# Kernel optimization log

Hardware: AMD Instinct MI355X
Metric: run time of the kernel (lower is better)

## Reference

```python
import jax, jax.numpy as jnp
import numpy as np

N_NODES = 50000
N_EDGES = 800000
N_GRAPHS = 128
IN_CH = 31
HID = 64
EPS = 1e-5


def _glorot(key, shape, scale=0.05):
    return jax.random.normal(key, shape, dtype=jnp.float32) * scale


def setup_inputs() -> dict:
    key = jax.random.key(0)
    ks = jax.random.split(key, 16)
    x = jax.random.normal(ks[0], (N_NODES, IN_CH), dtype=jnp.float32)
    edge_index = jax.random.randint(ks[1], (2, N_EDGES), 0, N_NODES, dtype=jnp.int32)
    batch = jnp.sort(jax.random.randint(ks[2], (N_NODES,), 0, N_GRAPHS, dtype=jnp.int32))
    params = {
        "t": jnp.ones((1,), dtype=jnp.float32),  # shared learnable softmax temperature
        "W1r": _glorot(ks[3], (HID, IN_CH)), "b1": jnp.zeros((HID,), jnp.float32), "W1s": _glorot(ks[4], (HID, IN_CH)),
        "W2r": _glorot(ks[5], (HID, HID)),  "b2": jnp.zeros((HID,), jnp.float32), "W2s": _glorot(ks[6], (HID, HID)),
        "W3r": _glorot(ks[7], (HID, HID)),  "b3": jnp.zeros((HID,), jnp.float32), "W3s": _glorot(ks[8], (HID, HID)),
        "Wl1": _glorot(ks[9], (2 * HID, 3 * HID)), "bl1": jnp.zeros((2 * HID,), jnp.float32),
        "Wl2": _glorot(ks[10], (HID // 2, 2 * HID)), "bl2": jnp.zeros((HID // 2,), jnp.float32),
    }
    return {"x": x, "edge_index": edge_index, "batch": batch, **params}


def _softmax_aggr(m, dst, t, n):
    # segment-softmax over incoming edges, per channel: alpha = softmax(t*m | dst)
    logits = m * t  # [E, C]
    mx = jax.ops.segment_max(logits, dst, num_segments=n)  # [N, C]
    e = jnp.exp(logits - mx[dst])
    denom = jax.ops.segment_sum(e, dst, num_segments=n)
    alpha = e / denom[dst]
    return jax.ops.segment_sum(m * alpha, dst, num_segments=n)  # [N, C]


def _graph_conv(x, src, dst, t, Wr, br, Ws):
    # PyG GraphConv: out = lin_rel(aggr_j x_j) + lin_root(x); lin_root has no bias
    m = x[src]  # gather [E, C]
    aggr = _softmax_aggr(m, dst, t, x.shape[0])
    return aggr @ Wr.T + br + x @ Ws.T


def _instance_norm(x):
    # torch InstanceNorm1d on [N, C] input -> normalize each row over feature dim
    mu = jnp.mean(x, axis=1, keepdims=True)
    var = jnp.mean((x - mu) ** 2, axis=1, keepdims=True)
    return (x - mu) / jnp.sqrt(var + EPS)


def reference(x, edge_index, batch, t, W1r, b1, W1s, W2r, b2, W2s, W3r, b3, W3s, Wl1, bl1, Wl2, bl2):
    src, dst = edge_index[0], edge_index[1]
    x1 = jax.nn.relu(_instance_norm(_graph_conv(x, src, dst, t, W1r, b1, W1s)))
    x2 = jax.nn.relu(_instance_norm(_graph_conv(x1, src, dst, t, W2r, b2, W2s)))
    x3 = jax.nn.relu(_instance_norm(_graph_conv(x2, src, dst, t, W3r, b3, W3s)))
    h1 = jax.ops.segment_max(x1, batch, num_segments=N_GRAPHS)
    h2 = jax.ops.segment_max(x2, batch, num_segments=N_GRAPHS)
    h3 = jax.ops.segment_max(x3, batch, num_segments=N_GRAPHS)
    h = jnp.concatenate([h1, h2, h3], axis=1)  # [G, 3*HID]
    z = jax.nn.relu(h @ Wl1.T + bl1)  # dropout is identity in eval mode
    z = z @ Wl2.T + bl2
    norm = jnp.maximum(jnp.linalg.norm(z, axis=1, keepdims=True), 1e-12)
    return z / norm
```

## Files before the change

### kernel.cpp

```cpp
#include <hip/hip_runtime.h>
#include <hip/hip_fp16.h>

#define N_NODES 50000
#define N_EDGES 800000
#define N_GRAPHS 128
#define IN_CH 31
#define HID 64

typedef __attribute__((ext_vector_type(8))) short short8;
typedef __attribute__((ext_vector_type(8))) unsigned short ushort8;
typedef __attribute__((ext_vector_type(4))) float floatx4;

__device__ inline unsigned f2bf(float f) {
    union { float f; unsigned u; } v; v.f = f;
    unsigned r = v.u + 0x7fff + ((v.u >> 16) & 1);
    return r >> 16;
}
__device__ inline void pack4(short* p, float4 v) {
    unsigned lo = f2bf(v.x) | (f2bf(v.y) << 16);
    unsigned hi = f2bf(v.z) | (f2bf(v.w) << 16);
    *(uint2*)p = make_uint2(lo, hi);
}
__device__ inline unsigned packEP(float E, float P) {
    __half2 h = __floats2half2_rn(E, P);
    return *(unsigned*)&h;
}
__device__ inline float2 unpackEP(unsigned u) {
    __half2 h = *(__half2*)&u;
    return __half22float2(h);
}

__global__ void prep_kernel(const float* __restrict__ x, const float* __restrict__ tptr,
                            unsigned short* __restrict__ xbf, unsigned* __restrict__ EP0,
                            int nN) {
    int i = blockIdx.x * 256 + threadIdx.x;
    if (i >= nN * 32) return;
    int node = i >> 5, c = i & 31;
    if (c < IN_CH) {
        float xv = x[node * IN_CH + c];
        xbf[node * IN_CH + c] = (unsigned short)f2bf(xv);
        float tval = tptr[0];
        float E = __expf(tval * xv);
        EP0[i] = packEP(E, xv * E);
    } else {
        EP0[i] = 0;
    }
}


#define BKT_SHIFT 7
#define BKT_MAX 512
#define CHUNK 8192
#define CAP 2560

__global__ void bucket_scatter_kernel(const int* __restrict__ src,
                                      const int* __restrict__ dst,
                                      int* __restrict__ bucket_cnt,
                                      unsigned* __restrict__ ebuf, int e, int nb) {
    __shared__ int bins[BKT_MAX];
    __shared__ int base[BKT_MAX];
    __shared__ int lcur[BKT_MAX];
    int tid = threadIdx.x;
    int i0 = blockIdx.x * CHUNK;
    int i1 = i0 + CHUNK; if (i1 > e) i1 = e;
    for (int k = tid; k < nb; k += 256) { bins[k] = 0; lcur[k] = 0; }
    __syncthreads();
    for (int j = i0 + tid; j < i1; j += 256)
        atomicAdd(&bins[dst[j] >> BKT_SHIFT], 1);
    __syncthreads();
    for (int k = tid; k < nb; k += 256)
        if (bins[k]) base[k] = atomicAdd(&bucket_cnt[k], bins[k]);
    __syncthreads();
    for (int j = i0 + tid; j < i1; j += 256) {
        int ss = src[j], dd = dst[j];
        int b = dd >> BKT_SHIFT;
        int p = atomicAdd(&lcur[b], 1);
        ebuf[(size_t)b * CAP + base[b] + p] = (unsigned)ss | ((unsigned)(dd & 127) << 16);
    }
}

__global__ void bucket_csr_kernel(const unsigned* __restrict__ ebuf,
                                  const int* __restrict__ bucket_cnt,
                                  int* __restrict__ row_ptr, int* __restrict__ deg,
                                  int* __restrict__ csr_src, int nN) {
    __shared__ int nh[128];
    __shared__ int s[128];
    __shared__ int ncur[128];
    int tid = threadIdx.x;
    int b = blockIdx.x;
    int cnt = bucket_cnt[b];
    size_t boff = (size_t)b * CAP;
    int node0 = b << BKT_SHIFT;
    if (tid < 128) nh[tid] = 0;
    __syncthreads();
    for (int j = tid; j < cnt; j += 256)
        atomicAdd(&nh[ebuf[boff + j] >> 16], 1);
    __syncthreads();
    int v = (tid < 128) ? nh[tid] : 0;
    if (tid < 128) s[tid] = v;
    __syncthreads();
    for (int off = 1; off < 128; off <<= 1) {
        int u = (tid < 128 && tid >= off) ? s[tid - off] : 0;
        __syncthreads();
        if (tid < 128) s[tid] += u;
        __syncthreads();
    }
    if (tid < 128 && node0 + tid < nN) {
        int excl = (int)boff + s[tid] - v;
        row_ptr[node0 + tid] = excl;
        deg[node0 + tid] = v;
        ncur[tid] = excl;
    }
    __syncthreads();
    for (int j = tid; j < cnt; j += 256) {
        unsigned ed = ebuf[boff + j];
        int pos = atomicAdd(&ncur[ed >> 16], 1);
        csr_src[pos] = (int)(ed & 0xFFFF);
    }
}


template <int C_IN>
__global__ void __launch_bounds__(256, 8) aggr_kernel(
        const unsigned* __restrict__ EP, const unsigned short* __restrict__ xin,
        const int* __restrict__ row_ptr, const int* __restrict__ deg,
        const int* __restrict__ csr_src,
        unsigned short* __restrict__ aRowsB, int n) {
    int w = threadIdx.x >> 6, l = threadIdx.x & 63;
    int d = blockIdx.x * 4 + w;
    if (d >= n) return;
    int beg = __builtin_amdgcn_readfirstlane(row_ptr[d]);
    int dg  = __builtin_amdgcn_readfirstlane(deg[d]);
    int end = beg + dg;
    int half = l >> 5;

    if constexpr (C_IN == 64) {
        int co = l & 31;
        float2 num2 = {0.f, 0.f}, den2 = {0.f, 0.f};
        int base = beg;
        for (; base + 64 <= end; base += 64) {
            int sidx = csr_src[base + l];
            #pragma unroll
            for (int j = 0; j < 64; j += 16) {
                uint2 v[8];
                #pragma unroll
                for (int p = 0; p < 8; ++p) {
                    int sa = __builtin_amdgcn_readlane(sidx, j + 2 * p);
                    int sb = __builtin_amdgcn_readlane(sidx, j + 2 * p + 1);
                    int s  = half ? sb : sa;
                    v[p] = *(const uint2*)&EP[(size_t)s * 64 + 2 * co];
                }
                #pragma unroll
                for (int p = 0; p < 8; ++p) {
                    float2 e0 = unpackEP(v[p].x);
                    float2 e1 = unpackEP(v[p].y);
                    den2.x += e0.x; num2.x += e0.y;
                    den2.y += e1.x; num2.y += e1.y;
                }
            }
        }
        int rem = end - base;
        if (rem > 0) {
            int sidx = csr_src[base + ((l < rem) ? l : 0)];
            for (int j = 0; j < rem; j += 16) {
                uint2 v[8];
                #pragma unroll
                for (int p = 0; p < 8; ++p) {
                    int ja = j + 2 * p;     if (ja >= rem) ja = rem - 1;
                    int jb = j + 2 * p + 1; if (jb >= rem) jb = rem - 1;
                    int sa = __builtin_amdgcn_readlane(sidx, ja);
                    int sb = __builtin_amdgcn_readlane(sidx, jb);
                    int s  = half ? sb : sa;
                    v[p] = *(const uint2*)&EP[(size_t)s * 64 + 2 * co];
                }
                #pragma unroll
                for (int p = 0; p < 8; ++p) {
                    float m = (j + 2 * p + half < rem) ? 1.f : 0.f;
                    float2 e0 = unpackEP(v[p].x);
                    float2 e1 = unpackEP(v[p].y);
                    den2.x = fmaf(e0.x, m, den2.x); num2.x = fmaf(e0.y, m, num2.x);
                    den2.y = fmaf(e1.x, m, den2.y); num2.y = fmaf(e1.y, m, num2.y);
                }
            }
        }
        num2.x += __shfl_xor(num2.x, 32);
        num2.y += __shfl_xor(num2.y, 32);
        den2.x += __shfl_xor(den2.x, 32);
        den2.y += __shfl_xor(den2.y, 32);
        float nx = __shfl(num2.x, l >> 1);
        float ny = __shfl(num2.y, l >> 1);
        float dx = __shfl(den2.x, l >> 1);
        float dy = __shfl(den2.y, l >> 1);
        float num = (l & 1) ? ny : nx;
        float den = (l & 1) ? dy : dx;
        float aggr = (dg > 0 && den > 0.f) ? num / den : 0.f;
        aRowsB[(size_t)d * 64 + l] = (unsigned short)f2bf(aggr);
    } else {
        int ch = l & 31;
        int chc = (ch < C_IN) ? ch : (C_IN - 1);
        float num = 0.f, den = 0.f;
        int base = beg;
        for (; base + 64 <= end; base += 64) {
            int sidx = csr_src[base + l];
            #pragma unroll
            for (int j = 0; j < 64; j += 16) {
                unsigned v[8];
                #pragma unroll
                for (int p = 0; p < 8; ++p) {
                    int sa = __builtin_amdgcn_readlane(sidx, j + 2 * p);
                    int sb = __builtin_amdgcn_readlane(sidx, j + 2 * p + 1);
                    int s  = half ? sb : sa;
                    v[p] = EP[(size_t)s * 32 + chc];
                }
                #pragma unroll
                for (int p = 0; p < 8; ++p) {
                    float2 e = unpackEP(v[p]);
                    den += e.x;
                    num += e.y;
                }
            }
        }
        int rem = end - base;
        if (rem > 0) {
            int sidx = csr_src[base + ((l < rem) ? l : 0)];
            for (int j = 0; j < rem; j += 16) {
                unsigned v[8];
                #pragma unroll
                for (int p = 0; p < 8; ++p) {
                    int ja = j + 2 * p;     if (ja >= rem) ja = rem - 1;
                    int jb = j + 2 * p + 1; if (jb >= rem) jb = rem - 1;
                    int sa = __builtin_amdgcn_readlane(sidx, ja);
                    int sb = __builtin_amdgcn_readlane(sidx, jb);
                    int s  = half ? sb : sa;
                    v[p] = EP[(size_t)s * 32 + chc];
                }
                #pragma unroll
                for (int p = 0; p < 8; ++p) {
                    float m = (j + 2 * p + half < rem) ? 1.f : 0.f;
                    float2 e = unpackEP(v[p]);
                    den = fmaf(e.x, m, den);
                    num = fmaf(e.y, m, num);
                }
            }
        }
        num += __shfl_xor(num, 32);
        den += __shfl_xor(den, 32);
        float aggr = (dg > 0 && den > 0.f) ? num / den : 0.f;
        unsigned short outv;
        if (l < C_IN)               outv = (unsigned short)f2bf(aggr);
        else if (l < 2 * C_IN)      outv = xin[(size_t)d * C_IN + (l - C_IN)];
        else                        outv = 0;
        aRowsB[(size_t)d * 64 + l] = outv;
    }
}


template <int C_IN, bool WEP>
__global__ void __launch_bounds__(256, 4) transform_kernel(
        const unsigned short* __restrict__ aRowsB, const unsigned short* __restrict__ yprev,
        const int* __restrict__ batch,
        const float* __restrict__ Wr, const float* __restrict__ br,
        const float* __restrict__ Ws, const float* __restrict__ tptr,
        unsigned short* __restrict__ yout, unsigned* __restrict__ EPout,
        float* __restrict__ hmax, int n) {
    constexpr int K_TOT = (C_IN == 64) ? 128 : 64;
    constexpr int KP    = K_TOT + 8;
    constexpr int KS    = K_TOT / 32;
    constexpr int ABSH  = 2 * 64 * KP;
    constexpr int CSH   = 64 * 68 * 2;
    constexpr int SMSH  = (ABSH > CSH) ? ABSH : CSH;

    __shared__ short smem[SMSH];
    short* sA = smem;
    short* sB = smem + 64 * KP;
    float* sC = (float*)smem;

    int tid = threadIdx.x;
    int nb = blockIdx.x * 64;

    if constexpr (C_IN == 64) {
        for (int idx = tid; idx < 64 * 16; idx += 256) {
            int row = idx >> 4, c8 = idx & 15;
            int node = nb + row; if (node >= n) node = n - 1;
            ushort8 v = (c8 < 8) ? ((const ushort8*)(aRowsB + (size_t)node * 64))[c8]
                                 : ((const ushort8*)(yprev + (size_t)node * 64))[c8 - 8];
            *(ushort8*)&sA[row * KP + c8 * 8] = v;
        }
        for (int idx = tid; idx < 64 * 32; idx += 256) {
            int nr = idx >> 5, c4 = idx & 31;
            float4 v = (c4 < 16) ? ((const float4*)(Wr + nr * 64))[c4]
                                 : ((const float4*)(Ws + nr * 64))[c4 - 16];
            pack4(&sB[nr * KP + c4 * 4], v);
        }
    } else {
        for (int idx = tid; idx < 64 * 8; idx += 256) {
            int row = idx >> 3, c8 = idx & 7;
            int node = nb + row; if (node >= n) node = n - 1;
            ushort8 v = ((const ushort8*)(aRowsB + (size_t)node * 64))[c8];
            *(ushort8*)&sA[row * KP + c8 * 8] = v;
        }
        for (int idx = tid; idx < 64 * 64; idx += 256) {
            int nr = idx >> 6, k = idx & 63;
            float v = (k < C_IN) ? Wr[nr * C_IN + k]
                    : (k < 2 * C_IN) ? Ws[nr * C_IN + (k - C_IN)] : 0.f;
            sB[nr * KP + k] = (short)f2bf(v);
        }
    }
    __syncthreads();

    int w = tid >> 6, l = tid & 63;
    int m = l & 15;
    int q = l >> 4;
    floatx4 acc[4] = {{0.f,0.f,0.f,0.f},{0.f,0.f,0.f,0.f},
                      {0.f,0.f,0.f,0.f},{0.f,0.f,0.f,0.f}};
    const short* aBase = &sA[(w * 16 + m) * KP + q * 8];
    #pragma unroll 2
    for (int s = 0; s < KS; ++s) {
        short8 af = *(const short8*)(aBase + s * 32);
        #pragma unroll
        for (int t = 0; t < 4; ++t) {
            short8 bf = *(const short8*)&sB[(t * 16 + m) * KP + q * 8 + s * 32];
            acc[t] = __builtin_amdgcn_mfma_f32_16x16x32_bf16(af, bf, acc[t], 0, 0, 0);
        }
    }

    __syncthreads();
    #pragma unroll
    for (int t = 0; t < 4; ++t)
        #pragma unroll
        for (int r = 0; r < 4; ++r)
            sC[(w * 16 + q * 4 + r) * 68 + t * 16 + m] = acc[t][r];
    __syncthreads();

    float bias = br[l];
    float tval = 0.f;
    if constexpr (WEP) tval = tptr[0];
    int gcur = -1;
    float rmax = 0.f;
    for (int i = 0; i < 16; ++i) {
        int j = w * 16 + i;
        int d = nb + j;
        if (d < n) {
            float a = sC[j * 68 + l] + bias;
            float s = a;
            for (int off = 32; off > 0; off >>= 1) s += __shfl_xor(s, off);
            float mu = s * (1.0f / 64.0f);
            float dc = a - mu;
            float s2 = dc * dc;
            for (int off = 32; off > 0; off >>= 1) s2 += __shfl_xor(s2, off);
            float var = s2 * (1.0f / 64.0f);
            float y = dc * rsqrtf(var + 1e-5f);
            y = fmaxf(y, 0.f);
            if constexpr (WEP) {
                yout[(size_t)d * 64 + l] = (unsigned short)f2bf(y);
                float E = __expf(tval * y);
                EPout[(size_t)d * 64 + l] = packEP(E, y * E);
            }
            int g = __builtin_amdgcn_readfirstlane(batch[d]);
            if (g != gcur) {
                if (gcur >= 0)
                    atomicMax((int*)&hmax[gcur * 64 + l], __float_as_int(rmax));
                gcur = g;
                rmax = 0.f;
            }
            rmax = fmaxf(rmax, y);
        }
    }
    if (gcur >= 0)
        atomicMax((int*)&hmax[gcur * 64 + l], __float_as_int(rmax));
}


__global__ void mlp_kernel(const float* __restrict__ h,
                           const float* __restrict__ Wl1, const float* __restrict__ bl1,
                           const float* __restrict__ Wl2, const float* __restrict__ bl2,
                           float* __restrict__ out) {
    __shared__ float hrow[192];
    __shared__ float z1[128];
    __shared__ float z2[32];
    __shared__ float snorm;
    int g = blockIdx.x, tid = threadIdx.x;
    if (tid < 64) {
        hrow[tid]       = h[0 * N_GRAPHS * 64 + g * 64 + tid];
        hrow[64 + tid]  = h[1 * N_GRAPHS * 64 + g * 64 + tid];
        hrow[128 + tid] = h[2 * N_GRAPHS * 64 + g * 64 + tid];
    }
    __syncthreads();
    float acc = bl1[tid];
    #pragma unroll 8
    for (int c = 0; c < 192; ++c) acc = fmaf(hrow[c], Wl1[tid * 192 + c], acc);
    z1[tid] = fmaxf(acc, 0.f);
    __syncthreads();
    if (tid < 32) {
        float a2 = bl2[tid];
        #pragma unroll 8
        for (int c = 0; c < 128; ++c) a2 = fmaf(z1[c], Wl2[tid * 128 + c], a2);
        z2[tid] = a2;
    }
    __syncthreads();
    if (tid == 0) {
        float ss = 0.f;
        for (int i = 0; i < 32; ++i) ss += z2[i] * z2[i];
        snorm = fmaxf(sqrtf(ss), 1e-12f);
    }
    __syncthreads();
    if (tid < 32) out[g * 32 + tid] = z2[tid] / snorm;
}


extern "C" void kernel_launch(void* const* d_in, const int* in_sizes, int n_in,
                              void* d_out, int out_size, void* d_ws, size_t ws_size,
                              hipStream_t stream) {
    const float* x   = (const float*)d_in[0];
    const int* eidx  = (const int*)d_in[1];
    const int* batch = (const int*)d_in[2];
    const float* t   = (const float*)d_in[3];
    const float* W1r = (const float*)d_in[4];
    const float* b1  = (const float*)d_in[5];
    const float* W1s = (const float*)d_in[6];
    const float* W2r = (const float*)d_in[7];
    const float* b2  = (const float*)d_in[8];
    const float* W2s = (const float*)d_in[9];
    const float* W3r = (const float*)d_in[10];
    const float* b3  = (const float*)d_in[11];
    const float* W3s = (const float*)d_in[12];
    const float* Wl1 = (const float*)d_in[13];
    const float* bl1 = (const float*)d_in[14];
    const float* Wl2 = (const float*)d_in[15];
    const float* bl2 = (const float*)d_in[16];
    float* out = (float*)d_out;

    const int nE = in_sizes[1] / 2;
    const int nN = in_sizes[2];
    const int* src = eidx;
    const int* dst = eidx + nE;
    const int nb = (nN + 127) >> BKT_SHIFT;

    char* ws = (char*)d_ws;
    size_t off = 0;
    auto alloc = [&](size_t bytes) {
        char* p = ws + off;
        off = (off + bytes + 255) & ~(size_t)255;
        return p;
    };
    int*            bucket_cnt = (int*)alloc((size_t)BKT_MAX * 4);
    float*          h          = (float*)alloc((size_t)3 * N_GRAPHS * 64 * 4);
    int*            row_ptr    = (int*)alloc((size_t)nN * 4);
    int*            deg        = (int*)alloc((size_t)nN * 4);
    unsigned*       ebuf       = (unsigned*)alloc((size_t)nb * CAP * 4);
    int*            csr_src    = (int*)alloc((size_t)nb * CAP * 4);
    unsigned short* xbf        = (unsigned short*)alloc((size_t)nN * IN_CH * 2);
    unsigned*       EP0        = (unsigned*)alloc((size_t)nN * 32 * 4);
    unsigned*       EPA        = (unsigned*)alloc((size_t)nN * 64 * 4);
    unsigned*       EPB        = (unsigned*)alloc((size_t)nN * 64 * 4);
    unsigned short* yAb        = (unsigned short*)alloc((size_t)nN * 64 * 2);
    unsigned short* yBb        = (unsigned short*)alloc((size_t)nN * 64 * 2);
    unsigned short* aRowsB     = (unsigned short*)alloc((size_t)nN * 64 * 2);

    const int nbChunk = (nE + CHUNK - 1) / CHUNK;

    hipMemsetAsync(bucket_cnt, 0,
                   (char*)(h + 3 * N_GRAPHS * 64) - (char*)bucket_cnt, stream);
    prep_kernel<<<(nN * 32 + 255) / 256, 256, 0, stream>>>(x, t, xbf, EP0, nN);
    bucket_scatter_kernel<<<nbChunk, 256, 0, stream>>>(src, dst, bucket_cnt, ebuf, nE, nb);
    bucket_csr_kernel<<<nb, 256, 0, stream>>>(ebuf, bucket_cnt, row_ptr, deg, csr_src, nN);

    const int nbA = (nN + 3) / 4;
    const int nbT = (nN + 63) / 64;

    aggr_kernel<IN_CH><<<nbA, 256, 0, stream>>>(EP0, xbf, row_ptr, deg, csr_src, aRowsB, nN);
    transform_kernel<IN_CH, true><<<nbT, 256, 0, stream>>>(
        aRowsB, nullptr, batch, W1r, b1, W1s, t, yAb, EPA, h + 0 * N_GRAPHS * 64, nN);

    aggr_kernel<HID><<<nbA, 256, 0, stream>>>(EPA, nullptr, row_ptr, deg, csr_src, aRowsB, nN);
    transform_kernel<HID, true><<<nbT, 256, 0, stream>>>(
        aRowsB, yAb, batch, W2r, b2, W2s, t, yBb, EPB, h + 1 * N_GRAPHS * 64, nN);

    aggr_kernel<HID><<<nbA, 256, 0, stream>>>(EPB, nullptr, row_ptr, deg, csr_src, aRowsB, nN);
    transform_kernel<HID, false><<<nbT, 256, 0, stream>>>(
        aRowsB, yBb, batch, W3r, b3, W3s, t, nullptr, nullptr, h + 2 * N_GRAPHS * 64, nN);

    mlp_kernel<<<N_GRAPHS, 128, 0, stream>>>(h, Wl1, bl1, Wl2, bl2, out);
}
```

Measured before the change: 274.4 us.

## Gather fp16 activations and recompute softmax exponentials in aggregation

Layers 2 and 3 no longer gather precomputed packed (exp, x*exp) pairs. They gather the fp16 activation rows and compute exp2(t*log2e*y) on the fly, which halves the bytes fetched per edge in the bandwidth-bound gather. The transform kernel also stops writing the EP buffers, and all storage and MFMA inputs switch from bf16 to fp16. The cost is more transcendental work per edge, plus fp16 range and precision risk in activations and weights.

```diff
diff --git a/kernel.cpp b/kernel.cpp
--- a/kernel.cpp
+++ b/kernel.cpp
@@ -10,20 +10,23 @@
 typedef __attribute__((ext_vector_type(8))) short short8;
 typedef __attribute__((ext_vector_type(8))) unsigned short ushort8;
 typedef __attribute__((ext_vector_type(4))) float floatx4;
-
-__device__ inline unsigned f2bf(float f) {
-    union { float f; unsigned u; } v; v.f = f;
-    unsigned r = v.u + 0x7fff + ((v.u >> 16) & 1);
-    return r >> 16;
-}
-__device__ inline void pack4(short* p, float4 v) {
-    unsigned lo = f2bf(v.x) | (f2bf(v.y) << 16);
-    unsigned hi = f2bf(v.z) | (f2bf(v.w) << 16);
+typedef __attribute__((ext_vector_type(8))) _Float16 half8;
+
+__device__ inline unsigned short f2h(float f) {
+    __half h = __float2half_rn(f);
+    return __half_as_ushort(h);
+}
+__device__ inline unsigned packh2(float a, float b) {
+    __half2 h = __floats2half2_rn(a, b);
+    return *(unsigned*)&h;
+}
+__device__ inline void pack4h(short* p, float4 v) {
+    unsigned lo = packh2(v.x, v.y);
+    unsigned hi = packh2(v.z, v.w);
     *(uint2*)p = make_uint2(lo, hi);
 }
 __device__ inline unsigned packEP(float E, float P) {
-    __half2 h = __floats2half2_rn(E, P);
-    return *(unsigned*)&h;
+    return packh2(E, P);
 }
 __device__ inline float2 unpackEP(unsigned u) {
     __half2 h = *(__half2*)&u;
@@ -31,14 +34,14 @@
 }
 
 __global__ void prep_kernel(const float* __restrict__ x, const float* __restrict__ tptr,
-                            unsigned short* __restrict__ xbf, unsigned* __restrict__ EP0,
+                            unsigned short* __restrict__ xh, unsigned* __restrict__ EP0,
                             int nN) {
     int i = blockIdx.x * 256 + threadIdx.x;
     if (i >= nN * 32) return;
     int node = i >> 5, c = i & 31;
     if (c < IN_CH) {
         float xv = x[node * IN_CH + c];
-        xbf[node * IN_CH + c] = (unsigned short)f2bf(xv);
+        xh[node * IN_CH + c] = f2h(xv);
         float tval = tptr[0];
         float E = __expf(tval * xv);
         EP0[i] = packEP(E, xv * E);
@@ -123,6 +126,7 @@
 template <int C_IN>
 __global__ void __launch_bounds__(256, 8) aggr_kernel(
         const unsigned* __restrict__ EP, const unsigned short* __restrict__ xin,
+        const float* __restrict__ tptr,
         const int* __restrict__ row_ptr, const int* __restrict__ deg,
         const int* __restrict__ csr_src,
         unsigned short* __restrict__ aRowsB, int n) {
@@ -136,26 +140,29 @@
 
     if constexpr (C_IN == 64) {
         int co = l & 31;
+        float t2 = tptr[0] * 1.44269504f;
+        const unsigned* Y = (const unsigned*)xin;
         float2 num2 = {0.f, 0.f}, den2 = {0.f, 0.f};
         int base = beg;
         for (; base + 64 <= end; base += 64) {
             int sidx = csr_src[base + l];
             #pragma unroll
             for (int j = 0; j < 64; j += 16) {
-                uint2 v[8];
+                unsigned v[8];
                 #pragma unroll
                 for (int p = 0; p < 8; ++p) {
                     int sa = __builtin_amdgcn_readlane(sidx, j + 2 * p);
                     int sb = __builtin_amdgcn_readlane(sidx, j + 2 * p + 1);
                     int s  = half ? sb : sa;
-                    v[p] = *(const uint2*)&EP[(size_t)s * 64 + 2 * co];
-                }
-                #pragma unroll
-                for (int p = 0; p < 8; ++p) {
-                    float2 e0 = unpackEP(v[p].x);
-                    float2 e1 = unpackEP(v[p].y);
-                    den2.x += e0.x; num2.x += e0.y;
-                    den2.y += e1.x; num2.y += e1.y;
+                    v[p] = Y[(size_t)s * 32 + co];
+                }
+                #pragma unroll
+                for (int p = 0; p < 8; ++p) {
+                    float2 y = __half22float2(*(__half2*)&v[p]);
+                    float E0 = exp2f(t2 * y.x);
+                    float E1 = exp2f(t2 * y.y);
+                    den2.x += E0; num2.x = fmaf(y.x, E0, num2.x);
+                    den2.y += E1; num2.y = fmaf(y.y, E1, num2.y);
                 }
             }
         }
@@ -163,7 +170,7 @@
         if (rem > 0) {
             int sidx = csr_src[base + ((l < rem) ? l : 0)];
             for (int j = 0; j < rem; j += 16) {
-                uint2 v[8];
+                unsigned v[8];
                 #pragma unroll
                 for (int p = 0; p < 8; ++p) {
                     int ja = j + 2 * p;     if (ja >= rem) ja = rem - 1;
@@ -171,15 +178,16 @@
                     int sa = __builtin_amdgcn_readlane(sidx, ja);
                     int sb = __builtin_amdgcn_readlane(sidx, jb);
                     int s  = half ? sb : sa;
-                    v[p] = *(const uint2*)&EP[(size_t)s * 64 + 2 * co];
+                    v[p] = Y[(size_t)s * 32 + co];
                 }
                 #pragma unroll
                 for (int p = 0; p < 8; ++p) {
                     float m = (j + 2 * p + half < rem) ? 1.f : 0.f;
-                    float2 e0 = unpackEP(v[p].x);
-                    float2 e1 = unpackEP(v[p].y);
-                    den2.x = fmaf(e0.x, m, den2.x); num2.x = fmaf(e0.y, m, num2.x);
-                    den2.y = fmaf(e1.x, m, den2.y); num2.y = fmaf(e1.y, m, num2.y);
+                    float2 y = __half22float2(*(__half2*)&v[p]);
+                    float E0 = exp2f(t2 * y.x);
+                    float E1 = exp2f(t2 * y.y);
+                    den2.x = fmaf(E0, m, den2.x); num2.x = fmaf(y.x * E0, m, num2.x);
+                    den2.y = fmaf(E1, m, den2.y); num2.y = fmaf(y.y * E1, m, num2.y);
                 }
             }
         }
@@ -194,7 +202,7 @@
         float num = (l & 1) ? ny : nx;
         float den = (l & 1) ? dy : dx;
         float aggr = (dg > 0 && den > 0.f) ? num / den : 0.f;
-        aRowsB[(size_t)d * 64 + l] = (unsigned short)f2bf(aggr);
+        aRowsB[(size_t)d * 64 + l] = f2h(aggr);
     } else {
         int ch = l & 31;
         int chc = (ch < C_IN) ? ch : (C_IN - 1);
@@ -247,7 +255,7 @@
         den += __shfl_xor(den, 32);
         float aggr = (dg > 0 && den > 0.f) ? num / den : 0.f;
         unsigned short outv;
-        if (l < C_IN)               outv = (unsigned short)f2bf(aggr);
+        if (l < C_IN)               outv = f2h(aggr);
         else if (l < 2 * C_IN)      outv = xin[(size_t)d * C_IN + (l - C_IN)];
         else                        outv = 0;
         aRowsB[(size_t)d * 64 + l] = outv;
@@ -255,13 +263,13 @@
 }
 
 
-template <int C_IN, bool WEP>
+template <int C_IN, bool WY>
 __global__ void __launch_bounds__(256, 4) transform_kernel(
         const unsigned short* __restrict__ aRowsB, const unsigned short* __restrict__ yprev,
         const int* __restrict__ batch,
         const float* __restrict__ Wr, const float* __restrict__ br,
-        const float* __restrict__ Ws, const float* __restrict__ tptr,
-        unsigned short* __restrict__ yout, unsigned* __restrict__ EPout,
+        const float* __restrict__ Ws,
+        unsigned short* __restrict__ yout,
         float* __restrict__ hmax, int n) {
     constexpr int K_TOT = (C_IN == 64) ? 128 : 64;
     constexpr int KP    = K_TOT + 8;
@@ -290,7 +298,7 @@
             int nr = idx >> 5, c4 = idx & 31;
             float4 v = (c4 < 16) ? ((const float4*)(Wr + nr * 64))[c4]
                                  : ((const float4*)(Ws + nr * 64))[c4 - 16];
-            pack4(&sB[nr * KP + c4 * 4], v);
+            pack4h(&sB[nr * KP + c4 * 4], v);
         }
     } else {
         for (int idx = tid; idx < 64 * 8; idx += 256) {
@@ -303,7 +311,7 @@
             int nr = idx >> 6, k = idx & 63;
             float v = (k < C_IN) ? Wr[nr * C_IN + k]
                     : (k < 2 * C_IN) ? Ws[nr * C_IN + (k - C_IN)] : 0.f;
-            sB[nr * KP + k] = (short)f2bf(v);
+            sB[nr * KP + k] = (short)f2h(v);
         }
     }
     __syncthreads();
@@ -316,11 +324,11 @@
     const short* aBase = &sA[(w * 16 + m) * KP + q * 8];
     #pragma unroll 2
     for (int s = 0; s < KS; ++s) {
-        short8 af = *(const short8*)(aBase + s * 32);
+        half8 af = *(const half8*)(aBase + s * 32);
         #pragma unroll
         for (int t = 0; t < 4; ++t) {
-            short8 bf = *(const short8*)&sB[(t * 16 + m) * KP + q * 8 + s * 32];
-            acc[t] = __builtin_amdgcn_mfma_f32_16x16x32_bf16(af, bf, acc[t], 0, 0, 0);
+            half8 bf = *(const half8*)&sB[(t * 16 + m) * KP + q * 8 + s * 32];
+            acc[t] = __builtin_amdgcn_mfma_f32_16x16x32_f16(af, bf, acc[t], 0, 0, 0);
         }
     }
 
@@ -333,8 +341,6 @@
     __syncthreads();
 
     float bias = br[l];
-    float tval = 0.f;
-    if constexpr (WEP) tval = tptr[0];
     int gcur = -1;
     float rmax = 0.f;
     for (int i = 0; i < 16; ++i) {
@@ -351,10 +357,8 @@
             float var = s2 * (1.0f / 64.0f);
             float y = dc * rsqrtf(var + 1e-5f);
             y = fmaxf(y, 0.f);
-            if constexpr (WEP) {
-                yout[(size_t)d * 64 + l] = (unsigned short)f2bf(y);
-                float E = __expf(tval * y);
-                EPout[(size_t)d * 64 + l] = packEP(E, y * E);
+            if constexpr (WY) {
+                yout[(size_t)d * 64 + l] = f2h(y);
             }
             int g = __builtin_amdgcn_readfirstlane(batch[d]);
             if (g != gcur) {
@@ -449,36 +453,34 @@
     int*            deg        = (int*)alloc((size_t)nN * 4);
     unsigned*       ebuf       = (unsigned*)alloc((size_t)nb * CAP * 4);
     int*            csr_src    = (int*)alloc((size_t)nb * CAP * 4);
-    unsigned short* xbf        = (unsigned short*)alloc((size_t)nN * IN_CH * 2);
+    unsigned short* xh         = (unsigned short*)alloc((size_t)nN * IN_CH * 2);
     unsigned*       EP0        = (unsigned*)alloc((size_t)nN * 32 * 4);
-    unsigned*       EPA        = (unsigned*)alloc((size_t)nN * 64 * 4);
-    unsigned*       EPB        = (unsigned*)alloc((size_t)nN * 64 * 4);
-    unsigned short* yAb        = (unsigned short*)alloc((size_t)nN * 64 * 2);
-    unsigned short* yBb        = (unsigned short*)alloc((size_t)nN * 64 * 2);
+    unsigned short* yAh        = (unsigned short*)alloc((size_t)nN * 64 * 2);
+    unsigned short* yBh        = (unsigned short*)alloc((size_t)nN * 64 * 2);
     unsigned short* aRowsB     = (unsigned short*)alloc((size_t)nN * 64 * 2);
 
     const int nbChunk = (nE + CHUNK - 1) / CHUNK;
 
     hipMemsetAsync(bucket_cnt, 0,
                    (char*)(h + 3 * N_GRAPHS * 64) - (char*)bucket_cnt, stream);
-    prep_kernel<<<(nN * 32 + 255) / 256, 256, 0, stream>>>(x, t, xbf, EP0, nN);
+    prep_kernel<<<(nN * 32 + 255) / 256, 256, 0, stream>>>(x, t, xh, EP0, nN);
     bucket_scatter_kernel<<<nbChunk, 256, 0, stream>>>(src, dst, bucket_cnt, ebuf, nE, nb);
     bucket_csr_kernel<<<nb, 256, 0, stream>>>(ebuf, bucket_cnt, row_ptr, deg, csr_src, nN);
 
     const int nbA = (nN + 3) / 4;
     const int nbT = (nN + 63) / 64;
 
-    aggr_kernel<IN_CH><<<nbA, 256, 0, stream>>>(EP0, xbf, row_ptr, deg, csr_src, aRowsB, nN);
+    aggr_kernel<IN_CH><<<nbA, 256, 0, stream>>>(EP0, xh, t, row_ptr, deg, csr_src, aRowsB, nN);
     transform_kernel<IN_CH, true><<<nbT, 256, 0, stream>>>(
-        aRowsB, nullptr, batch, W1r, b1, W1s, t, yAb, EPA, h + 0 * N_GRAPHS * 64, nN);
-
-    aggr_kernel<HID><<<nbA, 256, 0, stream>>>(EPA, nullptr, row_ptr, deg, csr_src, aRowsB, nN);
+        aRowsB, nullptr, batch, W1r, b1, W1s, yAh, h + 0 * N_GRAPHS * 64, nN);
+
+    aggr_kernel<HID><<<nbA, 256, 0, stream>>>(nullptr, yAh, t, row_ptr, deg, csr_src, aRowsB, nN);
     transform_kernel<HID, true><<<nbT, 256, 0, stream>>>(
-        aRowsB, yAb, batch, W2r, b2, W2s, t, yBb, EPB, h + 1 * N_GRAPHS * 64, nN);
-
-    aggr_kernel<HID><<<nbA, 256, 0, stream>>>(EPB, nullptr, row_ptr, deg, csr_src, aRowsB, nN);
+        aRowsB, yAh, batch, W2r, b2, W2s, yBh, h + 1 * N_GRAPHS * 64, nN);
+
+    aggr_kernel<HID><<<nbA, 256, 0, stream>>>(nullptr, yBh, t, row_ptr, deg, csr_src, aRowsB, nN);
     transform_kernel<HID, false><<<nbT, 256, 0, stream>>>(
-        aRowsB, yBb, batch, W3r, b3, W3s, t, nullptr, nullptr, h + 2 * N_GRAPHS * 64, nN);
+        aRowsB, yBh, batch, W3r, b3, W3s, nullptr, h + 2 * N_GRAPHS * 64, nN);
 
     mlp_kernel<<<N_GRAPHS, 128, 0, stream>>>(h, Wl1, bl1, Wl2, bl2, out);
 }
```

Measured after the change: 295.2 us. 1.08x slower.
